# Optimization experiments

Measured on AMD Instinct MI355X. Metric: run time of the kernel, lower is better.

The kernel has to match this reference:

```python
import jax, jax.numpy as jnp
import numpy as np

# ---- model hyperparameters (match init_kwargs) ----
D_MODEL = 1024
D_STATE = 128
EXPAND = 2
HEADDIM = 64
NGROUPS = 1
D_INNER = EXPAND * D_MODEL            # 2048
NHEADS = D_INNER // HEADDIM           # 32
ROPE_FRAC = 0.5
SPLIT = int(D_STATE * ROPE_FRAC)      # 64 rotary dims
NANG = SPLIT // 2                     # 32 rope angles
A_FLOOR = 1e-4
EPS = 1e-5
BATCH, SEQLEN = 1, 1024
SIZES = [D_INNER, D_INNER, D_STATE * NGROUPS, D_STATE * NGROUPS, NHEADS, NHEADS, NHEADS, NANG]
D_IN_PROJ = int(np.sum(SIZES))        # 4480


def setup_inputs() -> dict:
    key = jax.random.key(0)
    ks = jax.random.split(key, 6)
    u = jax.random.normal(ks[0], (BATCH, SEQLEN, D_MODEL), dtype=jnp.float32)
    W_in = jax.random.normal(ks[1], (D_MODEL, D_IN_PROJ), dtype=jnp.float32) * 0.02
    # dt_bias ~ log(dt) for dt in [1e-3, 0.1] -> around -4
    dt_bias = jax.random.normal(ks[2], (NHEADS,), dtype=jnp.float32) * 0.5 - 4.0
    B_bias = jnp.ones((NHEADS, D_STATE), jnp.float32) + 0.01 * jax.random.normal(ks[3], (NHEADS, D_STATE), dtype=jnp.float32)
    C_bias = jnp.ones((NHEADS, D_STATE), jnp.float32) + 0.01 * jax.random.normal(ks[4], (NHEADS, D_STATE), dtype=jnp.float32)
    Bn_w = jnp.ones((D_STATE,), jnp.float32)
    Cn_w = jnp.ones((D_STATE,), jnp.float32)
    D_param = jnp.ones((NHEADS,), jnp.float32)
    W_out = jax.random.normal(ks[5], (D_INNER, D_MODEL), dtype=jnp.float32) * 0.02
    return {"u": u, "W_in": W_in, "dt_bias": dt_bias, "B_bias": B_bias, "C_bias": C_bias,
            "Bn_w": Bn_w, "Cn_w": Cn_w, "D_param": D_param, "W_out": W_out}


def _rmsnorm(v, w):
    return v * jax.lax.rsqrt(jnp.mean(v * v, axis=-1, keepdims=True) + EPS) * w


def _forward(u, W_in, dt_bias, B_bias, C_bias, Bn_w, Cn_w, D_param, W_out):
    b, l, _ = u.shape
    proj = u @ W_in                                   # (b, l, d_in_proj)
    idx = np.cumsum(SIZES)[:-1]
    z, x, Bp, Cp, dd_dt, dd_A, trap_raw, ang = jnp.split(proj, idx, axis=-1)
    z = z.reshape(b, l, NHEADS, HEADDIM)
    x = x.reshape(b, l, NHEADS, HEADDIM)
    # A = clamp(-softplus(.), max=-A_floor);  dt = softplus(. + dt_bias)
    A = jnp.minimum(-jax.nn.softplus(dd_A), -A_FLOOR)          # (b,l,H)
    dt = jax.nn.softplus(dd_dt + dt_bias)                      # (b,l,H)
    a = jnp.exp(A * dt)                                        # decay per step
    lam = jax.nn.sigmoid(trap_raw)                             # trapezoid gate
    # RMSNorm on B/C (ngroups=1), then per-head additive bias
    Bn = _rmsnorm(Bp, Bn_w)                                    # (b,l,N)
    Cn = _rmsnorm(Cp, Cn_w)
    Bh = Bn[:, :, None, :] + B_bias                            # (b,l,H,N)
    Ch = Cn[:, :, None, :] + C_bias
    # data-dependent rotary: cumulative angle = cumsum(angles * dt)
    theta = jnp.cumsum(ang[:, :, None, :] * dt[..., None], axis=1)  # (b,l,H,NANG)
    cos, sin = jnp.cos(theta), jnp.sin(theta)

    def rope(v):
        d1, d2, rest = v[..., :NANG], v[..., NANG:SPLIT], v[..., SPLIT:]
        return jnp.concatenate([d1 * cos - d2 * sin, d1 * sin + d2 * cos, rest], axis=-1)

    Bh, Ch = rope(Bh), rope(Ch)

    tfirst = lambda v: jnp.moveaxis(v, 1, 0)
    inputs = (tfirst(Bh), tfirst(Ch), tfirst(x), tfirst(a), tfirst(dt), tfirst(lam))
    h0 = jnp.zeros((b, NHEADS, HEADDIM, D_STATE), jnp.float32)
    k0 = jnp.zeros((b, NHEADS, D_STATE), jnp.float32)
    v0 = jnp.zeros((b, NHEADS, HEADDIM), jnp.float32)

    def step(carry, inp):
        h, kp, vp = carry
        Bt, Ct, xt, at, dtt, lamt = inp
        # trapezoidal selective-scan update:
        # h_t = a_t h_{t-1} + dt_t (lam_t B_t x_t + (1-lam_t) a_t B_{t-1} x_{t-1})
        cur = jnp.einsum('bhp,bhn->bhpn', xt, Bt) * (dtt * lamt)[..., None, None]
        prv = jnp.einsum('bhp,bhn->bhpn', vp, kp) * (dtt * (1.0 - lamt) * at)[..., None, None]
        h = at[..., None, None] * h + cur + prv
        yt = jnp.einsum('bhn,bhpn->bhp', Ct, h)
        return (h, Bt, xt), yt

    _, y = jax.lax.scan(step, (h0, k0, v0), inputs)          # (l,b,H,P)
    y = jnp.moveaxis(y, 0, 1) + D_param[None, None, :, None] * x
    y = y * jax.nn.silu(z)                                    # gated output (no out-proj norm)
    return y.reshape(b, l, D_INNER) @ W_out


def reference(u, W_in, dt_bias, B_bias, C_bias, Bn_w, Cn_w, D_param, W_out):
    return _forward(u, W_in, dt_bias, B_bias, C_bias, Bn_w, Cn_w, D_param, W_out)
```

## Files before the change

kernel.cpp:

```cpp
#include <hip/hip_runtime.h>
#include <stdint.h>

#define SEQ     1024

typedef __attribute__((ext_vector_type(8))) short short8;
typedef __attribute__((ext_vector_type(4))) float f4;

__device__ __forceinline__ short f2b(float f){
  union { float f; uint32_t u; } v; v.f = f;
  uint32_t r = (v.u + 0x7fffu + ((v.u >> 16) & 1u)) >> 16;
  return (short)(uint16_t)r;
}
__device__ __forceinline__ float b2f(uint16_t u){
  union { uint32_t u; float f; } v; v.u = ((uint32_t)u) << 16; return v.f;
}
__device__ __forceinline__ uint32_t pack2(float lo, float hi){
  return (uint32_t)(uint16_t)f2b(lo) | ((uint32_t)(uint16_t)f2b(hi) << 16);
}
__device__ __forceinline__ float softplus_f(float x){
  return x > 20.f ? x : log1pf(__expf(x));
}
__device__ __forceinline__ void gload_lds16(const short* g, short* l){
  __builtin_amdgcn_global_load_lds((const __attribute__((address_space(1))) void*)g,
                                   (__attribute__((address_space(3))) void*)l, 16, 0, 0);
}

__global__ __launch_bounds__(256) void prep_inputs(const float* __restrict__ u, short* __restrict__ u16,
                                                   const float* __restrict__ W_in, short* __restrict__ WtIn,
                                                   const float* __restrict__ W_out, short* __restrict__ WtOut,
                                                   float* __restrict__ outz){
  int b = blockIdx.x;
  int tid = threadIdx.x;
  if (b < 1024){
    int i = (b * 256 + tid) * 4;
    f4 v = *(const f4*)(u + i);
    uint2 pk; pk.x = pack2(v.x, v.y); pk.y = pack2(v.z, v.w);
    *(uint2*)(u16 + i) = pk;
    return;
  }
  if (b >= 2656){
    int i = ((b - 2656) * 256 + tid) * 4;
    *(f4*)(outz + i) = (f4){0.f, 0.f, 0.f, 0.f};
    return;
  }
  const float* in; short* outp; int R, lda, bx, by;
  if (b < 2144){ int idx = b - 1024; bx = idx % 140; by = idx / 140; in = W_in;  outp = WtIn;  R = 1024; lda = 4480; }
  else         { int idx = b - 2144; bx = idx & 31;  by = idx >> 5;  in = W_out; outp = WtOut; R = 2048; lda = 1024; }
  __shared__ float tile[32][132];
  int bc = bx * 32, br = by * 128;
  int c = tid & 31, r0 = tid >> 5;
  #pragma unroll
  for (int i = 0; i < 16; i++){
    int r = r0 + i * 8;
    tile[c][r] = in[(size_t)(br + r) * lda + bc + c];
  }
  __syncthreads();
  #pragma unroll
  for (int i = 0; i < 4; i++){
    int task = tid + 256 * i;
    int cc = task >> 5;
    int rg = (task & 31) * 4;
    f4 v = *(const f4*)&tile[cc][rg];
    uint2 pk; pk.x = pack2(v.x, v.y); pk.y = pack2(v.z, v.w);
    *(uint2*)(outp + (size_t)(bc + cc) * R + br + rg) = pk;
  }
}

__global__ __launch_bounds__(256) void gemm1_kernel(const short* __restrict__ A, const short* __restrict__ Bt,
                                                    short* __restrict__ zx, short* __restrict__ xTb,
                                                    float* __restrict__ projT){
  const int K = 1024;
  __shared__ __align__(16) short As[2][128 * 32];
  __shared__ __align__(16) short Bs[2][160 * 32];
  const int tid  = threadIdx.x;
  const int wave = tid >> 6;
  const int lane = tid & 63;
  const int m0 = blockIdx.y * 128;
  const int n0 = blockIdx.x * 160;
  const int wm = (wave >> 1) * 64;
  const int wn = (wave & 1) * 80;
  const int quad = lane >> 4;
  const int r16  = lane & 15;

  f4 acc[4][5];
  #pragma unroll
  for (int i = 0; i < 4; i++)
    #pragma unroll
    for (int j = 0; j < 5; j++) acc[i][j] = (f4){0.f, 0.f, 0.f, 0.f};

  const int row0 = tid >> 2;
  const int kq   = tid & 3;
  const short* gA0 = A  + (size_t)(m0 + row0) * K + kq * 8;
  const short* gA1 = A  + (size_t)(m0 + row0 + 64) * K + kq * 8;
  const short* gB0 = Bt + (size_t)(n0 + row0) * K + kq * 8;
  const short* gB1 = Bt + (size_t)(n0 + row0 + 64) * K + kq * 8;
  const short* gB2 = Bt + (size_t)(n0 + row0 + 128) * K + kq * 8;

  gload_lds16(gA0, &As[0][(size_t)tid * 8]);
  gload_lds16(gA1, &As[0][(size_t)(tid + 256) * 8]);
  gload_lds16(gB0, &Bs[0][(size_t)tid * 8]);
  gload_lds16(gB1, &Bs[0][(size_t)(tid + 256) * 8]);
  if (tid < 128) gload_lds16(gB2, &Bs[0][(size_t)(tid + 512) * 8]);

  for (int kt = 0; kt < 32; ++kt){
    const int cur = kt & 1;
    __syncthreads();
    if (kt + 1 < 32){
      const int ko = (kt + 1) * 32;
      const int nxt = cur ^ 1;
      gload_lds16(gA0 + ko, &As[nxt][(size_t)tid * 8]);
      gload_lds16(gA1 + ko, &As[nxt][(size_t)(tid + 256) * 8]);
      gload_lds16(gB0 + ko, &Bs[nxt][(size_t)tid * 8]);
      gload_lds16(gB1 + ko, &Bs[nxt][(size_t)(tid + 256) * 8]);
      if (tid < 128) gload_lds16(gB2 + ko, &Bs[nxt][(size_t)(tid + 512) * 8]);
    }
    short8 af[4], bf[5];
    #pragma unroll
    for (int i = 0; i < 4; i++)
      af[i] = *(const short8*)&As[cur][(wm + i * 16 + r16) * 32 + quad * 8];
    #pragma unroll
    for (int j = 0; j < 5; j++)
      bf[j] = *(const short8*)&Bs[cur][(wn + j * 16 + r16) * 32 + quad * 8];
    #pragma unroll
    for (int i = 0; i < 4; i++)
      #pragma unroll
      for (int j = 0; j < 5; j++)
        acc[i][j] = __builtin_amdgcn_mfma_f32_16x16x32_bf16(af[i], bf[j], acc[i][j], 0, 0, 0);
  }

  #pragma unroll
  for (int i = 0; i < 4; i++)
    #pragma unroll
    for (int j = 0; j < 5; j++){
      int colb = n0 + wn + j * 16 + r16;
      int rowb = m0 + wm + i * 16 + quad * 4;
      if (colb < 2048){
        #pragma unroll
        for (int rr = 0; rr < 4; ++rr)
          zx[(size_t)(rowb + rr) * 4096 + colb] = f2b(acc[i][j][rr]);
      } else if (colb < 4096){
        uint2 pk; pk.x = pack2(acc[i][j][0], acc[i][j][1]); pk.y = pack2(acc[i][j][2], acc[i][j][3]);
        *(uint2*)(xTb + (size_t)(colb - 2048) * 1024 + rowb) = pk;
        #pragma unroll
        for (int rr = 0; rr < 4; ++rr)
          zx[(size_t)(rowb + rr) * 4096 + colb] = f2b(acc[i][j][rr]);
      } else {
        #pragma unroll
        for (int rr = 0; rr < 4; ++rr)
          projT[(size_t)(rowb + rr) * 384 + (colb - 4096)] = acc[i][j][rr];
      }
    }
}

__global__ __launch_bounds__(256) void gemm2_kernel(const short* __restrict__ A, const short* __restrict__ Bt,
                                                    float* __restrict__ C){
  const int N = 1024, K = 2048, klen = 512;
  __shared__ __align__(16) short As[2][128 * 32];
  __shared__ __align__(16) short Bs[2][128 * 32];
  const int tid  = threadIdx.x;
  const int wave = tid >> 6;
  const int lane = tid & 63;
  const int m0 = blockIdx.y * 128;
  const int n0 = blockIdx.x * 128;
  const int k0 = blockIdx.z * klen;
  const int wm = (wave >> 1) * 64;
  const int wn = (wave & 1) * 64;
  const int quad = lane >> 4;
  const int r16  = lane & 15;

  f4 acc[4][4];
  #pragma unroll
  for (int i = 0; i < 4; i++)
    #pragma unroll
    for (int j = 0; j < 4; j++) acc[i][j] = (f4){0.f, 0.f, 0.f, 0.f};

  const int row0 = tid >> 2;
  const int kq   = tid & 3;
  const short* gA0 = A  + (size_t)(m0 + row0) * K + k0 + kq * 8;
  const short* gA1 = A  + (size_t)(m0 + row0 + 64) * K + k0 + kq * 8;
  const short* gB0 = Bt + (size_t)(n0 + row0) * K + k0 + kq * 8;
  const short* gB1 = Bt + (size_t)(n0 + row0 + 64) * K + k0 + kq * 8;

  gload_lds16(gA0, &As[0][(size_t)tid * 8]);
  gload_lds16(gA1, &As[0][(size_t)(tid + 256) * 8]);
  gload_lds16(gB0, &Bs[0][(size_t)tid * 8]);
  gload_lds16(gB1, &Bs[0][(size_t)(tid + 256) * 8]);

  for (int kt = 0; kt < klen / 32; ++kt){
    const int cur = kt & 1;
    __syncthreads();
    if (kt + 1 < klen / 32){
      const int ko = (kt + 1) * 32;
      const int nxt = cur ^ 1;
      gload_lds16(gA0 + ko, &As[nxt][(size_t)tid * 8]);
      gload_lds16(gA1 + ko, &As[nxt][(size_t)(tid + 256) * 8]);
      gload_lds16(gB0 + ko, &Bs[nxt][(size_t)tid * 8]);
      gload_lds16(gB1 + ko, &Bs[nxt][(size_t)(tid + 256) * 8]);
    }
    short8 af[4], bf[4];
    #pragma unroll
    for (int i = 0; i < 4; i++){
      af[i] = *(const short8*)&As[cur][(wm + i * 16 + r16) * 32 + quad * 8];
      bf[i] = *(const short8*)&Bs[cur][(wn + i * 16 + r16) * 32 + quad * 8];
    }
    #pragma unroll
    for (int i = 0; i < 4; i++)
      #pragma unroll
      for (int j = 0; j < 4; j++)
        acc[i][j] = __builtin_amdgcn_mfma_f32_16x16x32_bf16(af[i], bf[j], acc[i][j], 0, 0, 0);
  }

  #pragma unroll
  for (int i = 0; i < 4; i++)
    #pragma unroll
    for (int j = 0; j < 4; j++)
      #pragma unroll
      for (int rr = 0; rr < 4; ++rr){
        int row = m0 + wm + i * 16 + quad * 4 + rr;
        int col = n0 + wn + j * 16 + r16;
        unsafeAtomicAdd(&C[(size_t)row * N + col], acc[i][j][rr]);
      }
}

__global__ __launch_bounds__(256) void scan_theta(const float* __restrict__ projT,
                                                  const float* __restrict__ dt_bias,
                                                  float* __restrict__ Lcum, float* __restrict__ u2b,
                                                  float* __restrict__ c1b,
                                                  float* __restrict__ cosb, float* __restrict__ sinb){
  int b = blockIdx.x;
  int tid = threadIdx.x;
  int t0 = tid * 4;
  int lane = tid & 63, wave = tid >> 6;
  __shared__ float wsum[4];
  if (b < 32){
    int h = b;
    float dtbias = dt_bias[h];
    float dt5[5], lam5[5];
    #pragma unroll
    for (int i = 0; i < 5; i++){
      int t = t0 + i;
      if (t < 1024){
        const float* row = projT + (size_t)t * 384;
        dt5[i]  = softplus_f(row[256 + h] + dtbias);
        lam5[i] = 1.f / (1.f + __expf(-row[320 + h]));
      } else { dt5[i] = 0.f; lam5[i] = 0.f; }
    }
    float v[4], c1[4], c2n[4];
    #pragma unroll
    for (int i = 0; i < 4; i++){
      int t = t0 + i;
      const float* row = projT + (size_t)t * 384;
      float Ah = -fmaxf(softplus_f(row[288 + h]), 1e-4f);
      v[i]   = Ah * dt5[i];
      c1[i]  = dt5[i] * lam5[i];
      c2n[i] = dt5[i + 1] * (1.f - lam5[i + 1]);
    }
    v[1] += v[0]; v[2] += v[1]; v[3] += v[2];
    float tot = v[3], sc = tot;
    #pragma unroll
    for (int off = 1; off < 64; off <<= 1){
      float n = __shfl_up(sc, off, 64);
      if (lane >= off) sc += n;
    }
    if (lane == 63) wsum[wave] = sc;
    __syncthreads();
    float base = sc - tot;
    for (int w = 0; w < wave; ++w) base += wsum[w];
    #pragma unroll
    for (int i = 0; i < 4; i++){
      int t = t0 + i;
      Lcum[h * 1024 + t] = base + v[i];
      u2b[h * 1024 + t]  = c1[i] + c2n[i];
      c1b[h * 1024 + t]  = c1[i];
    }
  } else {
    int hk = b - 32;
    int h = hk >> 5, k = hk & 31;
    float dtbias = dt_bias[h];
    float v[4];
    #pragma unroll
    for (int i = 0; i < 4; i++){
      const float* row = projT + (size_t)(t0 + i) * 384;
      float dt = softplus_f(row[256 + h] + dtbias);
      v[i] = row[352 + k] * dt;
    }
    v[1] += v[0]; v[2] += v[1]; v[3] += v[2];
    float tot = v[3], sc = tot;
    #pragma unroll
    for (int off = 1; off < 64; off <<= 1){
      float n = __shfl_up(sc, off, 64);
      if (lane >= off) sc += n;
    }
    if (lane == 63) wsum[wave] = sc;
    __syncthreads();
    float base = sc - tot;
    for (int w = 0; w < wave; ++w) base += wsum[w];
    #pragma unroll
    for (int i = 0; i < 4; i++){
      float th = base + v[i];
      float s, c;
      __sincosf(th, &s, &c);
      int t = t0 + i;
      cosb[(size_t)t * 1024 + h * 32 + k] = c;
      sinb[(size_t)t * 1024 + h * 32 + k] = s;
    }
  }
}

__global__ __launch_bounds__(256) void bcxt_kernel(const float* __restrict__ projT,
                                                   const float* __restrict__ B_bias, const float* __restrict__ C_bias,
                                                   const float* __restrict__ Bn_w, const float* __restrict__ Cn_w,
                                                   const float* __restrict__ cosb, const float* __restrict__ sinb,
                                                   short* __restrict__ Bb, short* __restrict__ Cb){
  int t = blockIdx.x;
  int tid = threadIdx.x;
  __shared__ float vv[2][128];
  __shared__ float red[4];
  int n = tid & 127;
  int isC = tid >> 7;
  float val = projT[(size_t)t * 384 + isC * 128 + n];
  float ss = val * val;
  #pragma unroll
  for (int off = 32; off >= 1; off >>= 1) ss += __shfl_down(ss, off);
  int wave = tid >> 6, lane = tid & 63;
  if (lane == 0) red[wave] = ss;
  __syncthreads();
  float rsv = isC ? rsqrtf((red[2] + red[3]) * (1.f / 128.f) + 1e-5f)
                  : rsqrtf((red[0] + red[1]) * (1.f / 128.f) + 1e-5f);
  vv[isC][n] = val * rsv * (isC ? Cn_w[n] : Bn_w[n]);
  __syncthreads();
  const float* cb = cosb + (size_t)t * 1024;
  const float* sb = sinb + (size_t)t * 1024;
  #pragma unroll
  for (int it = 0; it < 8; it++){
    int task = tid + 256 * it;
    int arr  = task >> 10;
    int rem  = task & 1023;
    int h    = rem >> 5;
    int n0   = (rem & 31) * 4;
    const float* bias = arr ? C_bias : B_bias;
    const float* base = vv[arr];
    f4 bv = *(const f4*)&base[n0];
    f4 bi = *(const f4*)&bias[h * 128 + n0];
    f4 o;
    if (n0 < 32){
      f4 bv2 = *(const f4*)&base[n0 + 32];
      f4 bi2 = *(const f4*)&bias[h * 128 + n0 + 32];
      f4 cv = *(const f4*)&cb[h * 32 + n0];
      f4 sv = *(const f4*)&sb[h * 32 + n0];
      #pragma unroll
      for (int q = 0; q < 4; q++) o[q] = (bv[q] + bi[q]) * cv[q] - (bv2[q] + bi2[q]) * sv[q];
    } else if (n0 < 64){
      int k0 = n0 - 32;
      f4 bv1 = *(const f4*)&base[k0];
      f4 bi1 = *(const f4*)&bias[h * 128 + k0];
      f4 cv = *(const f4*)&cb[h * 32 + k0];
      f4 sv = *(const f4*)&sb[h * 32 + k0];
      #pragma unroll
      for (int q = 0; q < 4; q++) o[q] = (bv1[q] + bi1[q]) * sv[q] + (bv[q] + bi[q]) * cv[q];
    } else {
      #pragma unroll
      for (int q = 0; q < 4; q++) o[q] = bv[q] + bi[q];
    }
    uint2 pk; pk.x = pack2(o.x, o.y); pk.y = pack2(o.z, o.w);
    short* outp = arr ? Cb : Bb;
    *(uint2*)(outp + (size_t)t * 4096 + h * 128 + n0) = pk;
  }
}

__global__ __launch_bounds__(256) void hpart_kernel(const short* __restrict__ xTb, const short* __restrict__ Bb,
                                                    const float* __restrict__ Lcum, const float* __restrict__ u2b,
                                                    short* __restrict__ Hpart){
  int h = blockIdx.x >> 3, c = blockIdx.x & 7;
  int t0 = c * 128;
  int tid = threadIdx.x;
  __shared__ float wS[128];
  if (tid < 128){
    float Lend = Lcum[h * 1024 + t0 + 127];
    wS[tid] = __expf(Lend - Lcum[h * 1024 + t0 + tid]) * u2b[h * 1024 + t0 + tid];
  }
  __syncthreads();
  int wave = tid >> 6, lane = tid & 63, quad = lane >> 4, r16 = lane & 15;
  int n0 = wave * 32;
  f4 acc[4][2];
  #pragma unroll
  for (int i = 0; i < 4; i++)
    #pragma unroll
    for (int j = 0; j < 2; j++) acc[i][j] = (f4){0.f, 0.f, 0.f, 0.f};

  const ushort* Bh = (const ushort*)Bb + (size_t)t0 * 4096 + h * 128;
  #pragma unroll
  for (int kk = 0; kk < 4; ++kk){
    int sb = kk * 32 + quad * 8;
    short8 af[4];
    #pragma unroll
    for (int i = 0; i < 4; i++){
      int p = i * 16 + r16;
      af[i] = *(const short8*)(xTb + (size_t)(h * 64 + p) * 1024 + t0 + sb);
    }
    float wv[8];
    #pragma unroll
    for (int jj = 0; jj < 8; jj++) wv[jj] = wS[sb + jj];
    short8 bfr[2];
    #pragma unroll
    for (int j = 0; j < 2; j++){
      int nn = n0 + j * 16 + r16;
      float e[8];
      #pragma unroll
      for (int jj = 0; jj < 8; jj++)
        e[jj] = b2f(Bh[(size_t)(sb + jj) * 4096 + nn]) * wv[jj];
      union { short8 s; uint32_t u[4]; } fr;
      #pragma unroll
      for (int q = 0; q < 4; q++) fr.u[q] = pack2(e[2 * q], e[2 * q + 1]);
      bfr[j] = fr.s;
    }
    #pragma unroll
    for (int i = 0; i < 4; i++)
      #pragma unroll
      for (int j = 0; j < 2; j++)
        acc[i][j] = __builtin_amdgcn_mfma_f32_16x16x32_bf16(af[i], bfr[j], acc[i][j], 0, 0, 0);
  }

  short* out = Hpart + ((size_t)(h * 8 + c)) * 8192;
  #pragma unroll
  for (int i = 0; i < 4; i++)
    #pragma unroll
    for (int rr = 0; rr < 4; ++rr){
      int p = i * 16 + quad * 4 + rr;
      #pragma unroll
      for (int j = 0; j < 2; j++){
        int nn = n0 + j * 16 + r16;
        out[p * 128 + nn] = f2b(acc[i][j][rr]);
      }
    }
}

#define GS 144
__global__ __launch_bounds__(256) void chunky_kernel(const short* __restrict__ Cb, const short* __restrict__ Bbg,
                                                     const short* __restrict__ xTb, const short* __restrict__ Hpart,
                                                     const float* __restrict__ Lcum, const float* __restrict__ u2b,
                                                     const float* __restrict__ c1b,
                                                     const short* __restrict__ zx, const float* __restrict__ D_par,
                                                     short* __restrict__ yb16){
  int h = blockIdx.x >> 3, c = blockIdx.x & 7;
  int t0 = c * 128;
  __shared__ __align__(16) short Gt[128 * GS];
  __shared__ __align__(16) short Hu[64 * 128];
  __shared__ float Lc[128], u2v[128], c1v[128];
  int tid = threadIdx.x;
  if (tid < 128){
    Lc[tid]  = Lcum[h * 1024 + t0 + tid];
    u2v[tid] = u2b[h * 1024 + t0 + tid];
    c1v[tid] = c1b[h * 1024 + t0 + tid];
  }
  float Lprev = (c > 0) ? Lcum[h * 1024 + t0 - 1] : 0.f;
  float Dp = D_par[h];

  {
    float hacc[32];
    #pragma unroll
    for (int q = 0; q < 32; q++) hacc[q] = 0.f;
    for (int cp = 0; cp < c; ++cp){
      float dec = __expf(Lprev - Lcum[h * 1024 + cp * 128 + 127]);
      const short8* hp = (const short8*)((const ushort*)Hpart + ((size_t)(h * 8 + cp)) * 8192 + tid * 32);
      #pragma unroll
      for (int q = 0; q < 4; q++){
        short8 v = hp[q];
        #pragma unroll
        for (int e = 0; e < 8; e++) hacc[q * 8 + e] += dec * b2f((uint16_t)v[e]);
      }
    }
    int p = tid >> 2;
    int wbase = tid * 64;
    #pragma unroll
    for (int q = 0; q < 4; q++){
      union { short8 s; uint32_t u[4]; } fr;
      #pragma unroll
      for (int p2 = 0; p2 < 4; p2++) fr.u[p2] = pack2(hacc[q * 8 + p2 * 2], hacc[q * 8 + p2 * 2 + 1]);
      int off = (wbase + q * 16) ^ ((p & 7) << 4);
      *(short8*)((char*)Hu + off) = fr.s;
    }
  }

  int wave = tid >> 6, lane = tid & 63, quad = lane >> 4, r16 = lane & 15;
  int wm = (wave >> 1) * 64, wn = (wave & 1) * 64;

  f4 acc[4][4];
  #pragma unroll
  for (int i = 0; i < 4; i++)
    #pragma unroll
    for (int j = 0; j < 4; j++) acc[i][j] = (f4){0.f, 0.f, 0.f, 0.f};
  #pragma unroll
  for (int kk = 0; kk < 4; ++kk){
    short8 af[4], bf[4];
    #pragma unroll
    for (int i = 0; i < 4; i++)
      af[i] = *(const short8*)(Cb + (size_t)(t0 + wm + i * 16 + r16) * 4096 + h * 128 + kk * 32 + quad * 8);
    #pragma unroll
    for (int j = 0; j < 4; j++)
      bf[j] = *(const short8*)(Bbg + (size_t)(t0 + wn + j * 16 + r16) * 4096 + h * 128 + kk * 32 + quad * 8);
    #pragma unroll
    for (int i = 0; i < 4; i++)
      #pragma unroll
      for (int j = 0; j < 4; j++)
        acc[i][j] = __builtin_amdgcn_mfma_f32_16x16x32_bf16(af[i], bf[j], acc[i][j], 0, 0, 0);
  }
  __syncthreads();

  #pragma unroll
  for (int i = 0; i < 4; i++){
    #pragma unroll
    for (int rr = 0; rr < 4; ++rr){
      int trow = wm + i * 16 + quad * 4 + rr;
      float Lt = Lc[trow];
      #pragma unroll
      for (int j = 0; j < 4; j++){
        int scol = wn + j * 16 + r16;
        float g = 0.f;
        if (scol <= trow){
          float wcoef = (scol == trow) ? c1v[scol] : u2v[scol];
          g = acc[i][j][rr] * wcoef * __expf(Lt - Lc[scol]);
        }
        Gt[trow * GS + scol] = f2b(g);
      }
    }
  }
  __syncthreads();

  f4 accY[2][4], accZ[2][4];
  #pragma unroll
  for (int i = 0; i < 2; i++)
    #pragma unroll
    for (int j = 0; j < 4; j++){ accY[i][j] = (f4){0.f,0.f,0.f,0.f}; accZ[i][j] = (f4){0.f,0.f,0.f,0.f}; }
  int m0 = wave * 32;
  #pragma unroll
  for (int kk = 0; kk < 4; ++kk){
    short8 ag[2], ac[2], bx[4], bh[4];
    #pragma unroll
    for (int i = 0; i < 2; i++){
      ag[i] = *(const short8*)&Gt[(m0 + i * 16 + r16) * GS + kk * 32 + quad * 8];
      ac[i] = *(const short8*)(Cb + (size_t)(t0 + m0 + i * 16 + r16) * 4096 + h * 128 + kk * 32 + quad * 8);
    }
    #pragma unroll
    for (int j = 0; j < 4; j++){
      bx[j] = *(const short8*)(xTb + (size_t)(h * 64 + j * 16 + r16) * 1024 + t0 + kk * 32 + quad * 8);
      int hrow = j * 16 + r16;
      int hoff = (hrow * 256 + kk * 64 + quad * 16) ^ ((hrow & 7) << 4);
      bh[j] = *(const short8*)((const char*)Hu + hoff);
    }
    #pragma unroll
    for (int i = 0; i < 2; i++)
      #pragma unroll
      for (int j = 0; j < 4; j++){
        accY[i][j] = __builtin_amdgcn_mfma_f32_16x16x32_bf16(ag[i], bx[j], accY[i][j], 0, 0, 0);
        accZ[i][j] = __builtin_amdgcn_mfma_f32_16x16x32_bf16(ac[i], bh[j], accZ[i][j], 0, 0, 0);
      }
  }
  const ushort* zxu = (const ushort*)zx;
  #pragma unroll
  for (int i = 0; i < 2; i++)
    #pragma unroll
    for (int rr = 0; rr < 4; ++rr){
      int trow = m0 + i * 16 + quad * 4 + rr;
      float ei = __expf(Lc[trow] - Lprev);
      const ushort* zrow = zxu + (size_t)(t0 + trow) * 4096;
      #pragma unroll
      for (int j = 0; j < 4; j++){
        int col = h * 64 + j * 16 + r16;
        float zv = b2f(zrow[col]);
        float xv = b2f(zrow[2048 + col]);
        float yv = accY[i][j][rr] + ei * accZ[i][j][rr] + Dp * xv;
        float o = yv * (zv / (1.f + __expf(-zv)));
        yb16[(size_t)(t0 + trow) * 2048 + col] = f2b(o);
      }
    }
}

extern "C" void kernel_launch(void* const* d_in, const int* in_sizes, int n_in,
                              void* d_out, int out_size, void* d_ws, size_t ws_size,
                              hipStream_t stream){
  const float* u       = (const float*)d_in[0];
  const float* W_in    = (const float*)d_in[1];
  const float* dt_bias = (const float*)d_in[2];
  const float* B_bias  = (const float*)d_in[3];
  const float* C_bias  = (const float*)d_in[4];
  const float* Bn_w    = (const float*)d_in[5];
  const float* Cn_w    = (const float*)d_in[6];
  const float* D_par   = (const float*)d_in[7];
  const float* W_out   = (const float*)d_in[8];
  float* out = (float*)d_out;

  char* ws = (char*)d_ws;
  short* u16   = (short*)(ws + 0);
  short* WtIn  = (short*)(ws + 2097152);
  short* WtOut = (short*)(ws + 11272192);
  short* zx    = (short*)(ws + 15466496);
  float* projT = (float*)(ws + 23855104);
  float* cosb  = (float*)(ws + 25427968);
  float* sinb  = (float*)(ws + 29622272);
  short* Bb    = (short*)(ws + 33816576);
  short* Cb    = (short*)(ws + 42205184);
  short* xTb   = (short*)(ws + 50593792);
  float* Lcum  = (float*)(ws + 54788096);
  float* u2b   = (float*)(ws + 54919168);
  float* c1b   = (float*)(ws + 55050240);
  short* Hpart = (short*)(ws + 55181312);
  short* yb16  = (short*)(ws + 59375616);

  prep_inputs<<<3680, 256, 0, stream>>>(u, u16, W_in, WtIn, W_out, WtOut, out);
  gemm1_kernel<<<dim3(28, 8), 256, 0, stream>>>(u16, WtIn, zx, xTb, projT);
  scan_theta<<<1056, 256, 0, stream>>>(projT, dt_bias, Lcum, u2b, c1b, cosb, sinb);
  bcxt_kernel<<<1024, 256, 0, stream>>>(projT, B_bias, C_bias, Bn_w, Cn_w, cosb, sinb, Bb, Cb);
  hpart_kernel<<<256, 256, 0, stream>>>(xTb, Bb, Lcum, u2b, Hpart);
  chunky_kernel<<<256, 256, 0, stream>>>(Cb, Bb, xTb, Hpart, Lcum, u2b, c1b, zx, D_par, yb16);
  gemm2_kernel<<<dim3(8, 8, 4), 256, 0, stream>>>(yb16, WtOut, out);
}
```

Before: 201.7 us.

## Fuse B/C prep, chunk-state and chunk-output kernels into one cooperative kernel

Merges bcxt, hpart and chunky into a single cooperative kernel. Each block builds its chunk's normalized, rotated B and C tiles directly in swizzled LDS, so the global Bb and Cb buffers and their round trips are gone. A grid-wide sync replaces the kernel boundary between the per-chunk state computation and the inter-chunk combine. This saves two launches and a lot of global traffic. In exchange it adds a grid barrier, about 90KB of LDS per block (lower occupancy), and a serial per-timestep loop for the B/C preprocessing.

```diff
diff --git a/kernel.cpp b/kernel.cpp
--- a/kernel.cpp
+++ b/kernel.cpp
@@ -1,4 +1,5 @@
 #include <hip/hip_runtime.h>
+#include <hip/hip_cooperative_groups.h>
 #include <stdint.h>
 
 #define SEQ     1024
@@ -23,6 +24,12 @@
 __device__ __forceinline__ void gload_lds16(const short* g, short* l){
   __builtin_amdgcn_global_load_lds((const __attribute__((address_space(1))) void*)g,
                                    (__attribute__((address_space(3))) void*)l, 16, 0, 0);
+}
+__device__ __forceinline__ short8 lds_read8(const short* base, int row, int bytecol){
+  return *(const short8*)((const char*)base + ((row * 256 + bytecol) ^ ((row & 7) << 4)));
+}
+__device__ __forceinline__ ushort lds_read2(const short* base, int row, int col){
+  return *(const ushort*)((const char*)base + ((row * 256 + col * 2) ^ ((row & 7) << 4)));
 }
 
 __global__ __launch_bounds__(256) void prep_inputs(const float* __restrict__ u, short* __restrict__ u16,
@@ -307,152 +314,145 @@
   }
 }
 
-__global__ __launch_bounds__(256) void bcxt_kernel(const float* __restrict__ projT,
+#define GS 144
+__global__ __launch_bounds__(256) void mega_kernel(const float* __restrict__ projT,
+                                                   const float* __restrict__ cosb, const float* __restrict__ sinb,
                                                    const float* __restrict__ B_bias, const float* __restrict__ C_bias,
                                                    const float* __restrict__ Bn_w, const float* __restrict__ Cn_w,
-                                                   const float* __restrict__ cosb, const float* __restrict__ sinb,
-                                                   short* __restrict__ Bb, short* __restrict__ Cb){
-  int t = blockIdx.x;
-  int tid = threadIdx.x;
-  __shared__ float vv[2][128];
-  __shared__ float red[4];
-  int n = tid & 127;
-  int isC = tid >> 7;
-  float val = projT[(size_t)t * 384 + isC * 128 + n];
-  float ss = val * val;
-  #pragma unroll
-  for (int off = 32; off >= 1; off >>= 1) ss += __shfl_down(ss, off);
-  int wave = tid >> 6, lane = tid & 63;
-  if (lane == 0) red[wave] = ss;
-  __syncthreads();
-  float rsv = isC ? rsqrtf((red[2] + red[3]) * (1.f / 128.f) + 1e-5f)
-                  : rsqrtf((red[0] + red[1]) * (1.f / 128.f) + 1e-5f);
-  vv[isC][n] = val * rsv * (isC ? Cn_w[n] : Bn_w[n]);
-  __syncthreads();
-  const float* cb = cosb + (size_t)t * 1024;
-  const float* sb = sinb + (size_t)t * 1024;
-  #pragma unroll
-  for (int it = 0; it < 8; it++){
-    int task = tid + 256 * it;
-    int arr  = task >> 10;
-    int rem  = task & 1023;
-    int h    = rem >> 5;
-    int n0   = (rem & 31) * 4;
-    const float* bias = arr ? C_bias : B_bias;
-    const float* base = vv[arr];
-    f4 bv = *(const f4*)&base[n0];
-    f4 bi = *(const f4*)&bias[h * 128 + n0];
-    f4 o;
-    if (n0 < 32){
-      f4 bv2 = *(const f4*)&base[n0 + 32];
-      f4 bi2 = *(const f4*)&bias[h * 128 + n0 + 32];
-      f4 cv = *(const f4*)&cb[h * 32 + n0];
-      f4 sv = *(const f4*)&sb[h * 32 + n0];
-      #pragma unroll
-      for (int q = 0; q < 4; q++) o[q] = (bv[q] + bi[q]) * cv[q] - (bv2[q] + bi2[q]) * sv[q];
-    } else if (n0 < 64){
-      int k0 = n0 - 32;
-      f4 bv1 = *(const f4*)&base[k0];
-      f4 bi1 = *(const f4*)&bias[h * 128 + k0];
-      f4 cv = *(const f4*)&cb[h * 32 + k0];
-      f4 sv = *(const f4*)&sb[h * 32 + k0];
-      #pragma unroll
-      for (int q = 0; q < 4; q++) o[q] = (bv1[q] + bi1[q]) * sv[q] + (bv[q] + bi[q]) * cv[q];
-    } else {
-      #pragma unroll
-      for (int q = 0; q < 4; q++) o[q] = bv[q] + bi[q];
-    }
-    uint2 pk; pk.x = pack2(o.x, o.y); pk.y = pack2(o.z, o.w);
-    short* outp = arr ? Cb : Bb;
-    *(uint2*)(outp + (size_t)t * 4096 + h * 128 + n0) = pk;
-  }
-}
-
-__global__ __launch_bounds__(256) void hpart_kernel(const short* __restrict__ xTb, const short* __restrict__ Bb,
-                                                    const float* __restrict__ Lcum, const float* __restrict__ u2b,
-                                                    short* __restrict__ Hpart){
+                                                   const short* __restrict__ xTb,
+                                                   const float* __restrict__ Lcum, const float* __restrict__ u2b,
+                                                   const float* __restrict__ c1b,
+                                                   const short* __restrict__ zx, const float* __restrict__ D_par,
+                                                   short* __restrict__ Hpart, short* __restrict__ yb16){
   int h = blockIdx.x >> 3, c = blockIdx.x & 7;
   int t0 = c * 128;
   int tid = threadIdx.x;
-  __shared__ float wS[128];
-  if (tid < 128){
+  int wave = tid >> 6, lane = tid & 63;
+  int quad = lane >> 4, r16 = lane & 15;
+
+  __shared__ __align__(16) short Bs[128 * 128];
+  __shared__ __align__(16) short Cs[128 * 128];
+  __shared__ __align__(16) short Gt[128 * GS];
+  __shared__ __align__(16) short Hu[64 * 128];
+  __shared__ float Lc[128], u2v[128], c1v[128], wS[128];
+
+  {
     float Lend = Lcum[h * 1024 + t0 + 127];
-    wS[tid] = __expf(Lend - Lcum[h * 1024 + t0 + tid]) * u2b[h * 1024 + t0 + tid];
+    if (tid < 128){
+      float lcv = Lcum[h * 1024 + t0 + tid];
+      float u2  = u2b[h * 1024 + t0 + tid];
+      Lc[tid] = lcv; u2v[tid] = u2; c1v[tid] = c1b[h * 1024 + t0 + tid];
+      wS[tid] = __expf(Lend - lcv) * u2;
+    }
+  }
+
+  {
+    float wBn0 = Bn_w[lane], wBn1 = Bn_w[64 + lane];
+    float wCn0 = Cn_w[lane], wCn1 = Cn_w[64 + lane];
+    float biB0 = B_bias[h * 128 + lane], biB1 = B_bias[h * 128 + 64 + lane];
+    float biC0 = C_bias[h * 128 + lane], biC1 = C_bias[h * 128 + 64 + lane];
+    float biBx = B_bias[h * 128 + (lane ^ 32)];
+    float biCx = C_bias[h * 128 + (lane ^ 32)];
+    int kang = lane & 31;
+    int tbase = wave * 32;
+    const float* pr = projT + (size_t)(t0 + tbase) * 384;
+    float pb0 = pr[lane], pb1 = pr[64 + lane], pc0 = pr[128 + lane], pc1 = pr[192 + lane];
+    float cv = cosb[(size_t)(t0 + tbase) * 1024 + h * 32 + kang];
+    float sv = sinb[(size_t)(t0 + tbase) * 1024 + h * 32 + kang];
+    for (int p = 0; p < 32; ++p){
+      int tloc = tbase + p;
+      float b0 = pb0, b1 = pb1, c0 = pc0, c1 = pc1, cvv = cv, svv = sv;
+      if (p + 1 < 32){
+        const float* pr2 = projT + (size_t)(t0 + tloc + 1) * 384;
+        pb0 = pr2[lane]; pb1 = pr2[64 + lane]; pc0 = pr2[128 + lane]; pc1 = pr2[192 + lane];
+        cv = cosb[(size_t)(t0 + tloc + 1) * 1024 + h * 32 + kang];
+        sv = sinb[(size_t)(t0 + tloc + 1) * 1024 + h * 32 + kang];
+      }
+      float sb = b0 * b0 + b1 * b1, sc = c0 * c0 + c1 * c1;
+      #pragma unroll
+      for (int off = 1; off < 64; off <<= 1){
+        sb += __shfl_xor(sb, off, 64);
+        sc += __shfl_xor(sc, off, 64);
+      }
+      float rb = rsqrtf(sb * (1.f / 128.f) + 1e-5f);
+      float rc = rsqrtf(sc * (1.f / 128.f) + 1e-5f);
+      float vB0 = b0 * rb * wBn0, vB1 = b1 * rb * wBn1;
+      float vC0 = c0 * rc * wCn0, vC1 = c1 * rc * wCn1;
+      float vBx = __shfl_xor(vB0, 32, 64), vCx = __shfl_xor(vC0, 32, 64);
+      float bb = vB0 + biB0, bbx = vBx + biBx;
+      float cb_ = vC0 + biC0, cbx = vCx + biCx;
+      float oB0 = (lane < 32) ? (bb * cvv - bbx * svv) : (bbx * svv + bb * cvv);
+      float oC0 = (lane < 32) ? (cb_ * cvv - cbx * svv) : (cbx * svv + cb_ * cvv);
+      float oB1 = vB1 + biB1;
+      float oC1 = vC1 + biC1;
+      int x1 = (tloc * 256 + lane * 2) ^ ((tloc & 7) << 4);
+      int x2 = (tloc * 256 + (64 + lane) * 2) ^ ((tloc & 7) << 4);
+      *(short*)((char*)Bs + x1) = f2b(oB0);
+      *(short*)((char*)Bs + x2) = f2b(oB1);
+      *(short*)((char*)Cs + x1) = f2b(oC0);
+      *(short*)((char*)Cs + x2) = f2b(oC1);
+    }
   }
   __syncthreads();
-  int wave = tid >> 6, lane = tid & 63, quad = lane >> 4, r16 = lane & 15;
-  int n0 = wave * 32;
-  f4 acc[4][2];
-  #pragma unroll
-  for (int i = 0; i < 4; i++)
-    #pragma unroll
-    for (int j = 0; j < 2; j++) acc[i][j] = (f4){0.f, 0.f, 0.f, 0.f};
-
-  const ushort* Bh = (const ushort*)Bb + (size_t)t0 * 4096 + h * 128;
-  #pragma unroll
-  for (int kk = 0; kk < 4; ++kk){
-    int sb = kk * 32 + quad * 8;
-    short8 af[4];
-    #pragma unroll
-    for (int i = 0; i < 4; i++){
-      int p = i * 16 + r16;
-      af[i] = *(const short8*)(xTb + (size_t)(h * 64 + p) * 1024 + t0 + sb);
-    }
-    float wv[8];
-    #pragma unroll
-    for (int jj = 0; jj < 8; jj++) wv[jj] = wS[sb + jj];
-    short8 bfr[2];
-    #pragma unroll
-    for (int j = 0; j < 2; j++){
-      int nn = n0 + j * 16 + r16;
-      float e[8];
-      #pragma unroll
-      for (int jj = 0; jj < 8; jj++)
-        e[jj] = b2f(Bh[(size_t)(sb + jj) * 4096 + nn]) * wv[jj];
-      union { short8 s; uint32_t u[4]; } fr;
-      #pragma unroll
-      for (int q = 0; q < 4; q++) fr.u[q] = pack2(e[2 * q], e[2 * q + 1]);
-      bfr[j] = fr.s;
-    }
+
+  {
+    int n0 = wave * 32;
+    f4 acc[4][2];
     #pragma unroll
     for (int i = 0; i < 4; i++)
       #pragma unroll
-      for (int j = 0; j < 2; j++)
-        acc[i][j] = __builtin_amdgcn_mfma_f32_16x16x32_bf16(af[i], bfr[j], acc[i][j], 0, 0, 0);
-  }
-
-  short* out = Hpart + ((size_t)(h * 8 + c)) * 8192;
-  #pragma unroll
-  for (int i = 0; i < 4; i++)
-    #pragma unroll
-    for (int rr = 0; rr < 4; ++rr){
-      int p = i * 16 + quad * 4 + rr;
+      for (int j = 0; j < 2; j++) acc[i][j] = (f4){0.f, 0.f, 0.f, 0.f};
+
+    #pragma unroll
+    for (int kk = 0; kk < 4; ++kk){
+      int sb = kk * 32 + quad * 8;
+      short8 af[4];
+      #pragma unroll
+      for (int i = 0; i < 4; i++){
+        int p = i * 16 + r16;
+        af[i] = *(const short8*)(xTb + (size_t)(h * 64 + p) * 1024 + t0 + sb);
+      }
+      float wv[8];
+      #pragma unroll
+      for (int jj = 0; jj < 8; jj++) wv[jj] = wS[sb + jj];
+      short8 bfr[2];
       #pragma unroll
       for (int j = 0; j < 2; j++){
         int nn = n0 + j * 16 + r16;
-        out[p * 128 + nn] = f2b(acc[i][j][rr]);
-      }
-    }
-}
-
-#define GS 144
-__global__ __launch_bounds__(256) void chunky_kernel(const short* __restrict__ Cb, const short* __restrict__ Bbg,
-                                                     const short* __restrict__ xTb, const short* __restrict__ Hpart,
-                                                     const float* __restrict__ Lcum, const float* __restrict__ u2b,
-                                                     const float* __restrict__ c1b,
-                                                     const short* __restrict__ zx, const float* __restrict__ D_par,
-                                                     short* __restrict__ yb16){
-  int h = blockIdx.x >> 3, c = blockIdx.x & 7;
-  int t0 = c * 128;
-  __shared__ __align__(16) short Gt[128 * GS];
-  __shared__ __align__(16) short Hu[64 * 128];
-  __shared__ float Lc[128], u2v[128], c1v[128];
-  int tid = threadIdx.x;
-  if (tid < 128){
-    Lc[tid]  = Lcum[h * 1024 + t0 + tid];
-    u2v[tid] = u2b[h * 1024 + t0 + tid];
-    c1v[tid] = c1b[h * 1024 + t0 + tid];
-  }
+        float e[8];
+        #pragma unroll
+        for (int jj = 0; jj < 8; jj++)
+          e[jj] = b2f(lds_read2(Bs, sb + jj, nn)) * wv[jj];
+        union { short8 s; uint32_t u[4]; } fr;
+        #pragma unroll
+        for (int q = 0; q < 4; q++) fr.u[q] = pack2(e[2 * q], e[2 * q + 1]);
+        bfr[j] = fr.s;
+      }
+      #pragma unroll
+      for (int i = 0; i < 4; i++)
+        #pragma unroll
+        for (int j = 0; j < 2; j++)
+          acc[i][j] = __builtin_amdgcn_mfma_f32_16x16x32_bf16(af[i], bfr[j], acc[i][j], 0, 0, 0);
+    }
+
+    if (c != 7){
+      short* outh = Hpart + ((size_t)(h * 8 + c)) * 8192;
+      #pragma unroll
+      for (int i = 0; i < 4; i++)
+        #pragma unroll
+        for (int rr = 0; rr < 4; ++rr){
+          int p = i * 16 + quad * 4 + rr;
+          #pragma unroll
+          for (int j = 0; j < 2; j++){
+            int nn = n0 + j * 16 + r16;
+            outh[p * 128 + nn] = f2b(acc[i][j][rr]);
+          }
+        }
+    }
+  }
+
+  cooperative_groups::this_grid().sync();
+
   float Lprev = (c > 0) ? Lcum[h * 1024 + t0 - 1] : 0.f;
   float Dp = D_par[h];
 
@@ -482,7 +482,6 @@
     }
   }
 
-  int wave = tid >> 6, lane = tid & 63, quad = lane >> 4, r16 = lane & 15;
   int wm = (wave >> 1) * 64, wn = (wave & 1) * 64;
 
   f4 acc[4][4];
@@ -492,13 +491,14 @@
     for (int j = 0; j < 4; j++) acc[i][j] = (f4){0.f, 0.f, 0.f, 0.f};
   #pragma unroll
   for (int kk = 0; kk < 4; ++kk){
+    int bc = kk * 64 + quad * 16;
     short8 af[4], bf[4];
     #pragma unroll
     for (int i = 0; i < 4; i++)
-      af[i] = *(const short8*)(Cb + (size_t)(t0 + wm + i * 16 + r16) * 4096 + h * 128 + kk * 32 + quad * 8);
+      af[i] = lds_read8(Cs, wm + i * 16 + r16, bc);
     #pragma unroll
     for (int j = 0; j < 4; j++)
-      bf[j] = *(const short8*)(Bbg + (size_t)(t0 + wn + j * 16 + r16) * 4096 + h * 128 + kk * 32 + quad * 8);
+      bf[j] = lds_read8(Bs, wn + j * 16 + r16, bc);
     #pragma unroll
     for (int i = 0; i < 4; i++)
       #pragma unroll
@@ -535,11 +535,12 @@
   int m0 = wave * 32;
   #pragma unroll
   for (int kk = 0; kk < 4; ++kk){
+    int bc = kk * 64 + quad * 16;
     short8 ag[2], ac[2], bx[4], bh[4];
     #pragma unroll
     for (int i = 0; i < 2; i++){
       ag[i] = *(const short8*)&Gt[(m0 + i * 16 + r16) * GS + kk * 32 + quad * 8];
-      ac[i] = *(const short8*)(Cb + (size_t)(t0 + m0 + i * 16 + r16) * 4096 + h * 128 + kk * 32 + quad * 8);
+      ac[i] = lds_read8(Cs, m0 + i * 16 + r16, bc);
     }
     #pragma unroll
     for (int j = 0; j < 4; j++){
@@ -598,20 +599,21 @@
   float* projT = (float*)(ws + 23855104);
   float* cosb  = (float*)(ws + 25427968);
   float* sinb  = (float*)(ws + 29622272);
-  short* Bb    = (short*)(ws + 33816576);
-  short* Cb    = (short*)(ws + 42205184);
-  short* xTb   = (short*)(ws + 50593792);
-  float* Lcum  = (float*)(ws + 54788096);
-  float* u2b   = (float*)(ws + 54919168);
-  float* c1b   = (float*)(ws + 55050240);
-  short* Hpart = (short*)(ws + 55181312);
-  short* yb16  = (short*)(ws + 59375616);
+  short* xTb   = (short*)(ws + 33816576);
+  float* Lcum  = (float*)(ws + 38010880);
+  float* u2b   = (float*)(ws + 38141952);
+  float* c1b   = (float*)(ws + 38273024);
+  short* Hpart = (short*)(ws + 38404096);
+  short* yb16  = (short*)(ws + 42598400);
 
   prep_inputs<<<3680, 256, 0, stream>>>(u, u16, W_in, WtIn, W_out, WtOut, out);
   gemm1_kernel<<<dim3(28, 8), 256, 0, stream>>>(u16, WtIn, zx, xTb, projT);
   scan_theta<<<1056, 256, 0, stream>>>(projT, dt_bias, Lcum, u2b, c1b, cosb, sinb);
-  bcxt_kernel<<<1024, 256, 0, stream>>>(projT, B_bias, C_bias, Bn_w, Cn_w, cosb, sinb, Bb, Cb);
-  hpart_kernel<<<256, 256, 0, stream>>>(xTb, Bb, Lcum, u2b, Hpart);
-  chunky_kernel<<<256, 256, 0, stream>>>(Cb, Bb, xTb, Hpart, Lcum, u2b, c1b, zx, D_par, yb16);
+
+  void* margs[] = { (void*)&projT, (void*)&cosb, (void*)&sinb, (void*)&B_bias, (void*)&C_bias,
+                    (void*)&Bn_w, (void*)&Cn_w, (void*)&xTb, (void*)&Lcum, (void*)&u2b,
+                    (void*)&c1b, (void*)&zx, (void*)&D_par, (void*)&Hpart, (void*)&yb16 };
+  hipLaunchCooperativeKernel((void*)mega_kernel, dim3(256), dim3(256), margs, 0, stream);
+
   gemm2_kernel<<<dim3(8, 8, 4), 256, 0, stream>>>(yb16, WtOut, out);
 }
```

Result: slower. 253.0 us (+25.4%).
